# Performance work log

Measured on AMD Instinct MI355X. Metric: run time of the kernel, lower is better.

The kernel has to match this reference:

```python
import jax, jax.numpy as jnp
import numpy as np

DN = ('NCHW', 'OIHW', 'NCHW')
WINDOW_SIZES = (11, 25, 49)


def conv(x, w, b=None, pad=0, groups=1):
    y = jax.lax.conv_general_dilated(
        x, w, window_strides=(1, 1), padding=((pad, pad), (pad, pad)),
        dimension_numbers=DN, feature_group_count=groups)
    if b is not None:
        y = y + b[None, :, None, None]
    return y


def box_mean(f, wsize):
    # depthwise box-filter local mean with reflect padding (matches F.pad mode='reflect')
    C = f.shape[1]
    p = wsize // 2
    fp = jnp.pad(f, ((0, 0), (0, 0), (p, p), (p, p)), mode='reflect')
    k = jnp.ones((C, 1, wsize, wsize), f.dtype) / (wsize * wsize)
    return conv(fp, k, groups=C)


def std_map(features, wsize):
    # per-channel local std, channel-weighted sum, then **0.8
    C = features.shape[1]
    # C == 8 here, so weights are softmax(ones) == uniform (torch path for C != 4)
    cw = jax.nn.softmax(jnp.ones((C,), features.dtype))
    m = box_mean(features, wsize)
    m2 = box_mean(features ** 2, wsize)
    var = jnp.clip(m2 - m ** 2, 1e-6, None)
    res = jnp.sum(cw[None, :, None, None] * jnp.sqrt(var), axis=1, keepdims=True)
    return res ** 0.8  # [B,1,H,W]


def setup_inputs() -> dict:
    key = jax.random.key(0)
    ks = jax.random.split(key, 8)
    B, C, H, W = 8, 4, 512, 512
    x = jax.random.normal(ks[0], (B, C, H, W), dtype=jnp.float32)
    conv1_w = jax.random.normal(ks[1], (32, 4, 3, 3), dtype=jnp.float32) * 0.1
    conv1_b = jnp.zeros((32,), jnp.float32)
    conv2_w = jax.random.normal(ks[2], (16, 32, 3, 3), dtype=jnp.float32) * 0.05
    conv2_b = jnp.zeros((16,), jnp.float32)
    conv3_w = jax.random.normal(ks[3], (8, 16, 3, 3), dtype=jnp.float32) * 0.05
    conv3_b = jnp.zeros((8,), jnp.float32)
    # scale_fusion init: weight = 1/len(window_sizes), bias = 0
    fusion_w = jnp.full((1, len(WINDOW_SIZES), 1, 1), 1.0 / len(WINDOW_SIZES), jnp.float32)
    fusion_b = jnp.zeros((1,), jnp.float32)
    channel_weights = jnp.ones((4,), jnp.float32) / 4.0
    return dict(x=x, conv1_w=conv1_w, conv1_b=conv1_b, conv2_w=conv2_w,
                conv2_b=conv2_b, conv3_w=conv3_w, conv3_b=conv3_b,
                fusion_w=fusion_w, fusion_b=fusion_b,
                channel_weights=channel_weights)


def reference(x, conv1_w, conv1_b, conv2_w, conv2_b, conv3_w, conv3_b,
              fusion_w, fusion_b, channel_weights):
    lrelu = lambda v: jnp.where(v >= 0, v, 0.2 * v)
    # feature extractor: conv3x3 -> lrelu -> conv3x3 -> lrelu -> conv3x3
    f = lrelu(conv(x, conv1_w, conv1_b, pad=1))
    f = lrelu(conv(f, conv2_w, conv2_b, pad=1))
    f = conv(f, conv3_w, conv3_b, pad=1)  # [B,8,H,W]
    # multi-scale std maps
    maps = [std_map(f, w) for w in WINDOW_SIZES]
    multi = jnp.concatenate(maps, axis=1)  # [B,3,H,W]
    fused = jax.nn.relu(conv(multi, fusion_w, fusion_b, pad=0))  # [B,1,H,W]
    # adaptive thresholds (global quantiles over the whole fused std map)
    qs = jnp.quantile(fused.reshape(-1), jnp.array([0.25, 0.75], fused.dtype))
    q25, q75 = qs[0], qs[1]
    iqr = q75 - q25
    gstd = jnp.std(x, axis=(2, 3), keepdims=True, ddof=1)  # [B,4,1,1] (torch unbiased)
    lo = (q25 - 0.5 * iqr) * jnp.ones_like(gstd)
    hi = (q75 + 0.5 * iqr) * jnp.ones_like(gstd)
    gf = jnp.clip(gstd * 5.0, 0.5, 2.0)
    lo, hi = lo * gf, hi * gf
    cw = jax.nn.softmax(channel_weights)[None, :, None, None]
    cstd = jnp.std(x * cw, axis=(2, 3), keepdims=True, ddof=1)
    cf = jnp.clip(cstd * 2.0, 0.8, 1.2)
    lo, hi = lo * cf, hi * cf
    # mask generation: broadcast [B,1,H,W] vs [B,4,1,1] -> [B,4,H,W], then mean over C
    n = jnp.clip((fused - lo) / (hi - lo), 0.0, 1.0)
    mask = jax.nn.sigmoid(6.0 * n - 3.0)
    return jnp.mean(mask, axis=1, keepdims=True)  # [B,1,H,W]
```

## Files before the change

### kernel.cpp

```cpp
#include <hip/hip_runtime.h>
#include <cmath>

#define HH 512
#define WW 512
#define NB 8
#define CIN 4
#define C2 32
#define C3 16
#define CF 8
#define HW (HH*WW)
#define NPIX (NB*HW)
#define NBC 2

__device__ __forceinline__ float lrelu_f(float v){ return v < 0.f ? 0.2f*v : v; }
__device__ __forceinline__ int reflect_i(int i){ int r = i < 0 ? -i : i; return r >= HH ? 2*HH - 2 - r : r; }

template<int Ci, int Co, bool LRELU>
__global__ __launch_bounds__(256) void k_conv8(const float* __restrict__ in,
                                               const float* __restrict__ wgt,
                                               const float* __restrict__ bias,
                                               float* __restrict__ outp)
{
    constexpr int NG = Co/8;
    __shared__ float wl[Co*Ci*9];
    __shared__ float bl[Co];
    for (int i = threadIdx.x; i < Co*Ci*9; i += 256) wl[i] = wgt[i];
    if (threadIdx.x < Co) bl[threadIdx.x] = bias[threadIdx.x];
    __syncthreads();

    int bid   = blockIdx.x;
    int local = bid % (NG*128);
    int b     = bid / (NG*128);
    int cb    = local & 3;
    int rb    = (local >> 2) & 31;
    int cg    = local >> 7;
    int tid   = threadIdx.x;
    int col   = cb*128 + (tid & 31)*4;
    int row0  = rb*16  + (tid >> 5)*2;
    int co0   = cg*8;
    const float* inb = in + (size_t)b*Ci*HW;

    float acc[8][2][4];
    #pragma unroll
    for (int j=0;j<8;j++){
        float bv = bl[co0+j];
        #pragma unroll
        for (int r=0;r<2;r++)
            #pragma unroll
            for (int p=0;p<4;p++) acc[j][r][p] = bv;
    }

    #pragma unroll 2
    for (int ci=0; ci<Ci; ci++){
        float v[4][6];
        const float* inc = inb + (size_t)ci*HW;
        #pragma unroll
        for (int dy=0;dy<4;dy++){
            int hh = row0 + dy - 1;
            int hc = hh < 0 ? 0 : (hh > HH-1 ? HH-1 : hh);
            bool hok = (unsigned)hh < (unsigned)HH;
            #pragma unroll
            for (int dx=0;dx<6;dx++){
                int wx = col + dx - 1;
                int wc = wx < 0 ? 0 : (wx > WW-1 ? WW-1 : wx);
                float val = inc[hc*WW + wc];
                v[dy][dx] = (hok && (unsigned)wx < (unsigned)WW) ? val : 0.f;
            }
        }
        #pragma unroll
        for (int j=0;j<8;j++){
            const float* wr = &wl[((co0+j)*Ci + ci)*9];
            float wj[9];
            #pragma unroll
            for (int q=0;q<9;q++) wj[q] = wr[q];
            #pragma unroll
            for (int dy=0;dy<3;dy++){
                #pragma unroll
                for (int dx=0;dx<3;dx++){
                    float wv = wj[dy*3+dx];
                    #pragma unroll
                    for (int r=0;r<2;r++)
                        #pragma unroll
                        for (int p=0;p<4;p++)
                            acc[j][r][p] = fmaf(v[dy+r][dx+p], wv, acc[j][r][p]);
                }
            }
        }
    }

    float* ob = outp + (size_t)b*Co*HW;
    #pragma unroll
    for (int j=0;j<8;j++){
        #pragma unroll
        for (int r=0;r<2;r++){
            float4 o;
            o.x = LRELU ? lrelu_f(acc[j][r][0]) : acc[j][r][0];
            o.y = LRELU ? lrelu_f(acc[j][r][1]) : acc[j][r][1];
            o.z = LRELU ? lrelu_f(acc[j][r][2]) : acc[j][r][2];
            o.w = LRELU ? lrelu_f(acc[j][r][3]) : acc[j][r][3];
            *(float4*)(ob + (size_t)(co0+j)*HW + (size_t)(row0+r)*WW + col) = o;
        }
    }
}

template<int WS>
__global__ __launch_bounds__(256) void k_vbox(const float* __restrict__ f,
                                              float* __restrict__ vs,
                                              float* __restrict__ vq)
{
    constexpr int P = WS/2;
    constexpr int CH = 64;
    int bid   = blockIdx.x;
    int wb    = bid & 1;
    int hc    = (bid >> 1) & 7;
    int plane = bid >> 4;
    int w     = wb*256 + threadIdx.x;
    int h0    = hc*CH;
    const float* base = f  + (size_t)plane*HW + w;
    float*       os   = vs + (size_t)plane*HW + w;
    float*       oq   = vq + (size_t)plane*HW + w;

    float s = 0.f, q = 0.f;
    #pragma unroll
    for (int dy = -P; dy <= P; dy++){
        float v = base[(size_t)reflect_i(h0+dy)*WW];
        s += v; q = fmaf(v, v, q);
    }
    #pragma unroll 4
    for (int h = h0; h < h0+CH; h++){
        os[(size_t)h*WW] = s;
        oq[(size_t)h*WW] = q;
        float e = base[(size_t)reflect_i(h+1+P)*WW];
        float l = base[(size_t)reflect_i(h-P)*WW];
        s += e - l;
        q = fmaf(e, e, q);
        q = fmaf(-l, l, q);
    }
}

__device__ __forceinline__ int swz_i(int j){ return j + (j >> 4); }

template<int WS>
__global__ __launch_bounds__(256) void k_hbox(const float* __restrict__ vs,
                                              const float* __restrict__ vq,
                                              float* __restrict__ fused,
                                              const float* __restrict__ fwv, int sidx)
{
    constexpr int P   = WS/2;
    constexpr int L   = WW + 2*P;
    constexpr int SWL = L + (L >> 4) + 2;
    constexpr float inv = 1.f/((float)WS*(float)WS);
    __shared__ float sv[CF*SWL];
    __shared__ float sq[CF*SWL];

    int bid = blockIdx.x;
    int row = bid & (HH-1);
    int bb  = bid >> 9;
    const float* vsb = vs + ((size_t)bb*CF*HH + row)*WW;
    const float* vqb = vq + ((size_t)bb*CF*HH + row)*WW;

    for (int i = threadIdx.x; i < CF*L; i += 256){
        int c = i / L, j = i - c*L;
        int s = j - P; s = s < 0 ? -s : (s > WW-1 ? 2*WW-2 - s : s);
        sv[c*SWL + swz_i(j)] = vsb[(size_t)c*HW + s];
        sq[c*SWL + swz_i(j)] = vqb[(size_t)c*HW + s];
    }
    __syncthreads();

    int c = threadIdx.x >> 5;
    int g = threadIdx.x & 31;
    const float* pv = sv + c*SWL;
    const float* pq = sq + c*SWL;
    int bofs = 17*g;

    float S = 0.f, Q = 0.f;
    #pragma unroll
    for (int k = 0; k < WS; k++){
        S += pv[bofs + k + (k>>4)];
        Q += pq[bofs + k + (k>>4)];
    }
    float res[16];
    #pragma unroll
    for (int k = 0; k < 16; k++){
        float m  = S*inv;
        float m2 = Q*inv;
        float var = fmaxf(fmaf(-m, m, m2), 1e-6f);
        res[k] = sqrtf(var);
        if (k < 15){
            S += pv[bofs + (k+WS) + ((k+WS)>>4)] - pv[bofs + k + (k>>4)];
            Q += pq[bofs + (k+WS) + ((k+WS)>>4)] - pq[bofs + k + (k>>4)];
        }
    }
    __syncthreads();
    #pragma unroll
    for (int k = 0; k < 16; k++) sv[c*SWL + bofs + k + (k>>4)] = res[k];
    __syncthreads();

    float fwb = fwv[sidx];
    #pragma unroll
    for (int half = 0; half < 2; half++){
        int col = threadIdx.x + half*256;
        float a = 0.f;
        #pragma unroll
        for (int cc = 0; cc < CF; cc++) a += sv[cc*SWL + swz_i(col)];
        float val = powf(a*0.125f, 0.8f);
        fused[((size_t)bb*HH + row)*WW + col] += fwb*val;
    }
}

__global__ void k_h8(const float* __restrict__ fused, const float* __restrict__ fb,
                     unsigned* __restrict__ hist8)
{
    __shared__ unsigned lh[256];
    lh[threadIdx.x] = 0;
    __syncthreads();
    float fbv = fb[0];
    int i = blockIdx.x*256 + threadIdx.x;
    int stride = gridDim.x*256;
    for (; i < NPIX; i += stride){
        float v = fmaxf(fused[i] + fbv, 0.f);
        atomicAdd(&lh[__float_as_uint(v) >> 24], 1u);
    }
    __syncthreads();
    if (lh[threadIdx.x]) atomicAdd(&hist8[threadIdx.x], lh[threadIdx.x]);
}

__global__ void k_scan8(const unsigned* __restrict__ hist8,
                        int* __restrict__ cand8, int* __restrict__ rank8)
{
    if (threadIdx.x == 0){
        const unsigned RK[4] = {524287u, 524288u, 1572863u, 1572864u};
        unsigned cum = 0; int qi = 0;
        for (int b = 0; b < 256 && qi < 4; b++){
            unsigned cnt = hist8[b];
            while (qi < 4 && RK[qi] < cum + cnt){
                cand8[qi] = b; rank8[qi] = (int)(RK[qi] - cum); qi++;
            }
            cum += cnt;
        }
    }
}

__global__ void k_h8b(const float* __restrict__ fused, const float* __restrict__ fb,
                      const int* __restrict__ cand8, unsigned* __restrict__ hist8b)
{
    __shared__ unsigned lh[1024];
    for (int i = threadIdx.x; i < 1024; i += 256) lh[i] = 0;
    __syncthreads();
    float fbv = fb[0];
    int c0 = cand8[0], c1 = cand8[1], c2 = cand8[2], c3 = cand8[3];
    bool d1 = (c1 != c0);
    bool d2 = (c2 != c0) && (c2 != c1);
    bool d3 = (c3 != c0) && (c3 != c1) && (c3 != c2);
    int i = blockIdx.x*256 + threadIdx.x;
    int stride = gridDim.x*256;
    for (; i < NPIX; i += stride){
        unsigned u = __float_as_uint(fmaxf(fused[i] + fbv, 0.f));
        int hi = (int)(u >> 24);
        unsigned mid = (u >> 16) & 0xffu;
        if (hi == c0)       atomicAdd(&lh[mid],       1u);
        if (d1 && hi == c1) atomicAdd(&lh[256u+mid],  1u);
        if (d2 && hi == c2) atomicAdd(&lh[512u+mid],  1u);
        if (d3 && hi == c3) atomicAdd(&lh[768u+mid],  1u);
    }
    __syncthreads();
    for (int i = threadIdx.x; i < 1024; i += 256)
        if (lh[i]) atomicAdd(&hist8b[i], lh[i]);
}

__global__ void k_scan8b(const unsigned* __restrict__ hist8b,
                         const int* __restrict__ cand8, const int* __restrict__ rank8,
                         int* __restrict__ cand16, int* __restrict__ rank16)
{
    int qi = threadIdx.x;
    if (qi < 4){
        int slot = qi;
        for (int j = 0; j < qi; j++) if (cand8[j] == cand8[qi]){ slot = j; break; }
        const unsigned* h = hist8b + slot*256;
        unsigned k = (unsigned)rank8[qi], cum = 0;
        for (int b = 0; b < 256; b++){
            unsigned cnt = h[b];
            if (cnt && k >= cum && k < cum + cnt){
                cand16[qi] = (cand8[qi] << 8) | b;
                rank16[qi] = (int)(k - cum);
            }
            cum += cnt;
        }
    }
}

__global__ void k_h16(const float* __restrict__ fused, const float* __restrict__ fb,
                      const int* __restrict__ cand16, unsigned* __restrict__ histlo)
{
    float fbv = fb[0];
    int c0 = cand16[0], c1 = cand16[1], c2 = cand16[2], c3 = cand16[3];
    bool d1 = (c1 != c0);
    bool d2 = (c2 != c0) && (c2 != c1);
    bool d3 = (c3 != c0) && (c3 != c1) && (c3 != c2);
    int i = blockIdx.x*256 + threadIdx.x;
    int stride = gridDim.x*256;
    for (; i < NPIX; i += stride){
        unsigned u = __float_as_uint(fmaxf(fused[i] + fbv, 0.f));
        int hi = (int)(u >> 16);
        unsigned lo = u & 0xffffu;
        if (hi == c0)       atomicAdd(&histlo[lo],           1u);
        if (d1 && hi == c1) atomicAdd(&histlo[65536u + lo],  1u);
        if (d2 && hi == c2) atomicAdd(&histlo[131072u + lo], 1u);
        if (d3 && hi == c3) atomicAdd(&histlo[196608u + lo], 1u);
    }
}

__global__ void k_scan16(const unsigned* __restrict__ histlo,
                         const int* __restrict__ cand16, const int* __restrict__ rank16,
                         float* __restrict__ ostat)
{
    int qi = blockIdx.x;
    int slot = qi;
    for (int j = 0; j < qi; j++) if (cand16[j] == cand16[qi]){ slot = j; break; }
    const unsigned* hist = histlo + (size_t)slot*65536;
    __shared__ unsigned csum[256];
    __shared__ unsigned cbase[256];
    int t = threadIdx.x;
    unsigned s = 0;
    for (int i = 0; i < 256; i++) s += hist[t*256 + i];
    csum[t] = s;
    __syncthreads();
    if (t == 0){ unsigned run = 0; for (int i = 0; i < 256; i++){ cbase[i] = run; run += csum[i]; } }
    __syncthreads();
    unsigned k = (unsigned)rank16[qi];
    unsigned cum = cbase[t];
    for (int i = 0; i < 256; i++){
        unsigned cnt = hist[t*256 + i];
        if (cnt && k >= cum && k < cum + cnt)
            ostat[qi] = __uint_as_float(((unsigned)cand16[qi] << 16) | (unsigned)(t*256 + i));
        cum += cnt;
    }
}

__global__ void k_gstd_part(const float* __restrict__ x, double* __restrict__ part)
{
    int bid = blockIdx.x;
    int plane = bid >> 3, chunk = bid & 7;
    const float4* p4 = (const float4*)(x + (size_t)plane*HW + (size_t)chunk*32768);
    int t = threadIdx.x;
    double s=0.0, s2=0.0;
    for (int k=0;k<32;k++){
        float4 v = p4[k*256 + t];
        s  += (double)v.x + (double)v.y + (double)v.z + (double)v.w;
        s2 += (double)v.x*v.x + (double)v.y*v.y + (double)v.z*v.z + (double)v.w*v.w;
    }
    __shared__ double rs[256], rq[256];
    rs[t]=s; rq[t]=s2; __syncthreads();
    for (int off=128; off>0; off>>=1){
        if (t<off){ rs[t]+=rs[t+off]; rq[t]+=rq[t+off]; }
        __syncthreads();
    }
    if (t==0){ part[bid*2]=rs[0]; part[bid*2+1]=rq[0]; }
}

__global__ void k_gstd_final(const double* __restrict__ part, float* __restrict__ gstd)
{
    int t = threadIdx.x;
    if (t < 32){
        double s=0.0, s2=0.0;
        for (int j=0;j<8;j++){ s += part[(t*8+j)*2]; s2 += part[(t*8+j)*2+1]; }
        const double N = 262144.0;
        double var = (s2 - s*s/N) / (N - 1.0);
        gstd[t] = (float)sqrt(var < 0.0 ? 0.0 : var);
    }
}

__global__ void k_finalize(const float* __restrict__ ostat, const float* __restrict__ gstd,
                           const float* __restrict__ cwin, float* __restrict__ lov, float* __restrict__ hiv)
{
    int t = threadIdx.x;
    if (t < 32){
        float q25 = ostat[0] + 0.75f*(ostat[1]-ostat[0]);
        float q75 = ostat[2] + 0.25f*(ostat[3]-ostat[2]);
        float iqr = q75 - q25;
        float lo_b = q25 - 0.5f*iqr, hi_b = q75 + 0.5f*iqr;
        int c = t & 3;
        float m = fmaxf(fmaxf(cwin[0],cwin[1]), fmaxf(cwin[2],cwin[3]));
        float e0 = expf(cwin[0]-m), e1 = expf(cwin[1]-m), e2 = expf(cwin[2]-m), e3 = expf(cwin[3]-m);
        float smc = expf(cwin[c]-m) / (e0+e1+e2+e3);
        float g  = gstd[t];
        float gf = fminf(fmaxf(g*5.f, 0.5f), 2.f);
        float cf = fminf(fmaxf(smc*g*2.f, 0.8f), 1.2f);
        lov[t] = lo_b*gf*cf;
        hiv[t] = hi_b*gf*cf;
    }
}

__global__ void k_mask(const float* __restrict__ fused_in, const float* __restrict__ fb,
                       const float* __restrict__ lov, const float* __restrict__ hiv,
                       float* __restrict__ outp)
{
    int i = blockIdx.x*256 + threadIdx.x;
    float F = fmaxf(fused_in[i] + fb[0], 0.f);
    int b = i >> 18;
    float o = 0.f;
    #pragma unroll
    for (int c=0;c<4;c++){
        float lo = lov[b*4+c], hi = hiv[b*4+c];
        float n = (F - lo) / (hi - lo);
        n = fminf(fmaxf(n, 0.f), 1.f);
        o += 1.f/(1.f + expf(3.f - 6.f*n));
    }
    outp[i] = 0.25f * o;
}

extern "C" void kernel_launch(void* const* d_in, const int* in_sizes, int n_in,
                              void* d_out, int out_size, void* d_ws, size_t ws_size,
                              hipStream_t stream)
{
    const float* x  = (const float*)d_in[0];
    const float* w1 = (const float*)d_in[1];
    const float* b1 = (const float*)d_in[2];
    const float* w2 = (const float*)d_in[3];
    const float* b2 = (const float*)d_in[4];
    const float* w3 = (const float*)d_in[5];
    const float* b3 = (const float*)d_in[6];
    const float* fw = (const float*)d_in[7];
    const float* fb = (const float*)d_in[8];
    const float* cw = (const float*)d_in[9];
    float* out = (float*)d_out;
    char* ws = (char*)d_ws;

    size_t off = 0;
    auto take = [&](size_t bytes)->size_t{ size_t o = off; off += (bytes + 255) & ~(size_t)255; return o; };
    size_t o_h8     = take(256*4);
    size_t o_h8b    = take(1024*4);
    size_t o_histlo = take((size_t)4*65536*4);
    size_t o_c8     = take(4*4);
    size_t o_r8     = take(4*4);
    size_t o_c16    = take(4*4);
    size_t o_r16    = take(4*4);
    size_t o_os     = take(4*4);
    size_t o_part   = take(512*8);
    size_t o_gs     = take(32*4);
    size_t o_lo     = take(32*4);
    size_t o_hi     = take(32*4);
    size_t o_R1     = take((size_t)NB*C3*HW*4);
    size_t o_R2     = take((size_t)NBC*C2*HW*4);

    float*    f2buf  = (float*)(ws + o_R1);
    float*    vsb    = (float*)(ws + o_R1);
    float*    vqb    = vsb + (size_t)NB*CF*HW;
    float*    f1     = (float*)(ws + o_R2);
    float*    fbuf   = (float*)(ws + o_R2);
    unsigned* hist8  = (unsigned*)(ws + o_h8);
    unsigned* hist8b = (unsigned*)(ws + o_h8b);
    unsigned* histlo = (unsigned*)(ws + o_histlo);
    int*      c8     = (int*)(ws + o_c8);
    int*      r8     = (int*)(ws + o_r8);
    int*      c16    = (int*)(ws + o_c16);
    int*      r16    = (int*)(ws + o_r16);
    float*    osv    = (float*)(ws + o_os);
    double*   part   = (double*)(ws + o_part);
    float*    gs     = (float*)(ws + o_gs);
    float*    lov    = (float*)(ws + o_lo);
    float*    hiv    = (float*)(ws + o_hi);

    for (int ck = 0; ck < NB/NBC; ck++){
        const float* xb = x + (size_t)ck*NBC*CIN*HW;
        k_conv8<CIN,C2,true ><<<NBC*512,256,0,stream>>>(xb, w1, b1, f1);
        k_conv8<C2, C3,true ><<<NBC*256,256,0,stream>>>(f1, w2, b2,
                                                        f2buf + (size_t)ck*NBC*C3*HW);
    }
    k_conv8<C3, CF, false><<<NB*128,256,0,stream>>>(f2buf, w3, b3, fbuf);

    k_gstd_part<<<256,256,0,stream>>>(x, part);
    k_gstd_final<<<1,256,0,stream>>>(part, gs);

    hipMemsetAsync(out, 0, (size_t)NPIX*4, stream);
    const int vgrid = NB*CF*16, hgrid = NB*512;
    k_vbox<11><<<vgrid,256,0,stream>>>(fbuf, vsb, vqb);
    k_hbox<11><<<hgrid,256,0,stream>>>(vsb, vqb, out, fw, 0);
    k_vbox<25><<<vgrid,256,0,stream>>>(fbuf, vsb, vqb);
    k_hbox<25><<<hgrid,256,0,stream>>>(vsb, vqb, out, fw, 1);
    k_vbox<49><<<vgrid,256,0,stream>>>(fbuf, vsb, vqb);
    k_hbox<49><<<hgrid,256,0,stream>>>(vsb, vqb, out, fw, 2);

    hipMemsetAsync(hist8,  0, 256*4,  stream);
    hipMemsetAsync(hist8b, 0, 1024*4, stream);
    hipMemsetAsync(histlo, 0, (size_t)4*65536*4, stream);
    k_h8    <<<2048,256,0,stream>>>(out, fb, hist8);
    k_scan8 <<<1,64,0,stream>>>(hist8, c8, r8);
    k_h8b   <<<2048,256,0,stream>>>(out, fb, c8, hist8b);
    k_scan8b<<<1,64,0,stream>>>(hist8b, c8, r8, c16, r16);
    k_h16   <<<2048,256,0,stream>>>(out, fb, c16, histlo);
    k_scan16<<<4,256,0,stream>>>(histlo, c16, r16, osv);

    k_finalize<<<1,64,0,stream>>>(osv, gs, cw, lov, hiv);
    k_mask<<<NPIX/256,256,0,stream>>>(out, fb, lov, hiv, out);
}
```

Measured before the change: 916.7 us.

## Fuse vertical and horizontal box filters into one tiled kernel; shuffle conv halos

The separate vertical-sum and horizontal-sum kernels, which wrote intermediate vs/vq planes to global memory, are replaced by one kernel per window size. Each block owns a 16-row by 256-column band, keeps running vertical sums in registers and does the horizontal sliding sums from shared memory, so the large intermediate buffers and the output memset go away. The 3x3 conv input load now uses a float4 per row plus wave shuffles for the halo columns instead of six scalar loads. The trade-off is a small grid (512 blocks) with a __syncthreads-heavy per-row loop and uncoalesced reflected column gathers, which may reduce occupancy and parallelism.

```diff
diff --git a/kernel.cpp b/kernel.cpp
--- a/kernel.cpp
+++ b/kernel.cpp
@@ -35,7 +35,8 @@
     int rb    = (local >> 2) & 31;
     int cg    = local >> 7;
     int tid   = threadIdx.x;
-    int col   = cb*128 + (tid & 31)*4;
+    int lane  = tid & 31;
+    int col   = cb*128 + lane*4;
     int row0  = rb*16  + (tid >> 5)*2;
     int co0   = cg*8;
     const float* inb = in + (size_t)b*Ci*HW;
@@ -59,13 +60,18 @@
             int hh = row0 + dy - 1;
             int hc = hh < 0 ? 0 : (hh > HH-1 ? HH-1 : hh);
             bool hok = (unsigned)hh < (unsigned)HH;
-            #pragma unroll
-            for (int dx=0;dx<6;dx++){
-                int wx = col + dx - 1;
-                int wc = wx < 0 ? 0 : (wx > WW-1 ? WW-1 : wx);
-                float val = inc[hc*WW + wc];
-                v[dy][dx] = (hok && (unsigned)wx < (unsigned)WW) ? val : 0.f;
-            }
+            const float* rowp = inc + hc*WW;
+            float4 m = *(const float4*)(rowp + col);
+            float lft = 0.f, rgt = 0.f;
+            if (lane == 0  && col > 0)      lft = rowp[col-1];
+            if (lane == 31 && col+4 < WW)   rgt = rowp[col+4];
+            float v0 = __shfl_up(m.w, 1, 32);
+            float v5 = __shfl_down(m.x, 1, 32);
+            if (lane == 0)  v0 = lft;
+            if (lane == 31) v5 = rgt;
+            if (!hok){ m.x=0.f; m.y=0.f; m.z=0.f; m.w=0.f; v0=0.f; v5=0.f; }
+            v[dy][0]=v0; v[dy][1]=m.x; v[dy][2]=m.y;
+            v[dy][3]=m.z; v[dy][4]=m.w; v[dy][5]=v5;
         }
         #pragma unroll
         for (int j=0;j<8;j++){
@@ -103,108 +109,113 @@
     }
 }
 
-template<int WS>
-__global__ __launch_bounds__(256) void k_vbox(const float* __restrict__ f,
-                                              float* __restrict__ vs,
-                                              float* __restrict__ vq)
-{
-    constexpr int P = WS/2;
-    constexpr int CH = 64;
-    int bid   = blockIdx.x;
-    int wb    = bid & 1;
-    int hc    = (bid >> 1) & 7;
-    int plane = bid >> 4;
-    int w     = wb*256 + threadIdx.x;
-    int h0    = hc*CH;
-    const float* base = f  + (size_t)plane*HW + w;
-    float*       os   = vs + (size_t)plane*HW + w;
-    float*       oq   = vq + (size_t)plane*HW + w;
-
-    float s = 0.f, q = 0.f;
+template<int WS, bool FIRST>
+__global__ __launch_bounds__(256) void k_vhbox(const float* __restrict__ f,
+                                               float* __restrict__ fused,
+                                               const float* __restrict__ fwv, int sidx)
+{
+    constexpr int P    = WS/2;
+    constexpr int SW   = ((256 + 2*P + 31)/32)*32;
+    constexpr int SEGC = SW/32;
+    constexpr int SVW  = (SW + (SW>>4) + 3) | 1;
+    constexpr int RSW  = 256 + 16 + 2;
+    constexpr float inv = 1.f/((float)WS*(float)WS);
+
+    __shared__ float sv[CF*SVW];
+    __shared__ float sq[CF*SVW];
+    __shared__ float resv[CF*RSW];
+
+    int bid  = blockIdx.x;
+    int band = bid & 31;
+    int half = (bid >> 5) & 1;
+    int b    = bid >> 6;
+    int r0   = band*16;
+    int c0   = half*256;
+    int tid  = threadIdx.x;
+    int ch   = tid >> 5;
+    int seg  = tid & 31;
+
+    const float* fp = f + (size_t)(b*CF + ch)*HW;
+
+    int rc[SEGC];
     #pragma unroll
+    for (int k = 0; k < SEGC; k++){
+        int gc = c0 - P + k*32 + seg;
+        gc = gc < 0 ? -gc : (gc > WW-1 ? 2*WW-2 - gc : gc);
+        rc[k] = gc;
+    }
+
+    float vsr[SEGC], vqr[SEGC];
+    #pragma unroll
+    for (int k = 0; k < SEGC; k++){ vsr[k]=0.f; vqr[k]=0.f; }
     for (int dy = -P; dy <= P; dy++){
-        float v = base[(size_t)reflect_i(h0+dy)*WW];
-        s += v; q = fmaf(v, v, q);
-    }
-    #pragma unroll 4
-    for (int h = h0; h < h0+CH; h++){
-        os[(size_t)h*WW] = s;
-        oq[(size_t)h*WW] = q;
-        float e = base[(size_t)reflect_i(h+1+P)*WW];
-        float l = base[(size_t)reflect_i(h-P)*WW];
-        s += e - l;
-        q = fmaf(e, e, q);
-        q = fmaf(-l, l, q);
-    }
-}
-
-__device__ __forceinline__ int swz_i(int j){ return j + (j >> 4); }
-
-template<int WS>
-__global__ __launch_bounds__(256) void k_hbox(const float* __restrict__ vs,
-                                              const float* __restrict__ vq,
-                                              float* __restrict__ fused,
-                                              const float* __restrict__ fwv, int sidx)
-{
-    constexpr int P   = WS/2;
-    constexpr int L   = WW + 2*P;
-    constexpr int SWL = L + (L >> 4) + 2;
-    constexpr float inv = 1.f/((float)WS*(float)WS);
-    __shared__ float sv[CF*SWL];
-    __shared__ float sq[CF*SWL];
-
-    int bid = blockIdx.x;
-    int row = bid & (HH-1);
-    int bb  = bid >> 9;
-    const float* vsb = vs + ((size_t)bb*CF*HH + row)*WW;
-    const float* vqb = vq + ((size_t)bb*CF*HH + row)*WW;
-
-    for (int i = threadIdx.x; i < CF*L; i += 256){
-        int c = i / L, j = i - c*L;
-        int s = j - P; s = s < 0 ? -s : (s > WW-1 ? 2*WW-2 - s : s);
-        sv[c*SWL + swz_i(j)] = vsb[(size_t)c*HW + s];
-        sq[c*SWL + swz_i(j)] = vqb[(size_t)c*HW + s];
-    }
-    __syncthreads();
-
-    int c = threadIdx.x >> 5;
-    int g = threadIdx.x & 31;
-    const float* pv = sv + c*SWL;
-    const float* pq = sq + c*SWL;
-    int bofs = 17*g;
-
-    float S = 0.f, Q = 0.f;
-    #pragma unroll
-    for (int k = 0; k < WS; k++){
-        S += pv[bofs + k + (k>>4)];
-        Q += pq[bofs + k + (k>>4)];
-    }
-    float res[16];
-    #pragma unroll
-    for (int k = 0; k < 16; k++){
-        float m  = S*inv;
-        float m2 = Q*inv;
-        float var = fmaxf(fmaf(-m, m, m2), 1e-6f);
-        res[k] = sqrtf(var);
-        if (k < 15){
-            S += pv[bofs + (k+WS) + ((k+WS)>>4)] - pv[bofs + k + (k>>4)];
-            Q += pq[bofs + (k+WS) + ((k+WS)>>4)] - pq[bofs + k + (k>>4)];
-        }
-    }
-    __syncthreads();
-    #pragma unroll
-    for (int k = 0; k < 16; k++) sv[c*SWL + bofs + k + (k>>4)] = res[k];
-    __syncthreads();
+        const float* rp = fp + (size_t)reflect_i(r0+dy)*WW;
+        #pragma unroll
+        for (int k = 0; k < SEGC; k++){
+            float v = rp[rc[k]];
+            vsr[k] += v; vqr[k] = fmaf(v, v, vqr[k]);
+        }
+    }
 
     float fwb = fwv[sidx];
-    #pragma unroll
-    for (int half = 0; half < 2; half++){
-        int col = threadIdx.x + half*256;
+
+    for (int rr = 0; rr < 16; rr++){
+        __syncthreads();
+        #pragma unroll
+        for (int k = 0; k < SEGC; k++){
+            int j = k*32 + seg; int sj = j + (j>>4);
+            sv[ch*SVW + sj] = vsr[k];
+            sq[ch*SVW + sj] = vqr[k];
+        }
+        float ev[SEGC], lv[SEGC];
+        if (rr < 15){
+            const float* ep = fp + (size_t)reflect_i(r0+rr+1+P)*WW;
+            const float* lp = fp + (size_t)reflect_i(r0+rr-P)*WW;
+            #pragma unroll
+            for (int k = 0; k < SEGC; k++){ ev[k]=ep[rc[k]]; lv[k]=lp[rc[k]]; }
+        }
+        __syncthreads();
+        int oc0 = seg*8;
+        float S = 0.f, Q = 0.f;
+        #pragma unroll
+        for (int k = 0; k < WS; k++){
+            int j = oc0 + k; int sj = j + (j>>4);
+            S += sv[ch*SVW + sj];
+            Q += sq[ch*SVW + sj];
+        }
+        float res[8];
+        #pragma unroll
+        for (int t = 0; t < 8; t++){
+            float m  = S*inv, m2 = Q*inv;
+            float var = fmaxf(fmaf(-m, m, m2), 1e-6f);
+            res[t] = sqrtf(var);
+            if (t < 7){
+                int ja = oc0 + t + WS, jb = oc0 + t;
+                S += sv[ch*SVW + ja + (ja>>4)] - sv[ch*SVW + jb + (jb>>4)];
+                Q += sq[ch*SVW + ja + (ja>>4)] - sq[ch*SVW + jb + (jb>>4)];
+            }
+        }
+        #pragma unroll
+        for (int t = 0; t < 8; t++){
+            int j = oc0 + t;
+            resv[ch*RSW + j + (j>>4)] = res[t];
+        }
+        if (rr < 15){
+            #pragma unroll
+            for (int k = 0; k < SEGC; k++){
+                vsr[k] += ev[k] - lv[k];
+                vqr[k] = fmaf(ev[k], ev[k], vqr[k]);
+                vqr[k] = fmaf(-lv[k], lv[k], vqr[k]);
+            }
+        }
+        __syncthreads();
+        int colI = tid;
         float a = 0.f;
         #pragma unroll
-        for (int cc = 0; cc < CF; cc++) a += sv[cc*SWL + swz_i(col)];
-        float val = powf(a*0.125f, 0.8f);
-        fused[((size_t)bb*HH + row)*WW + col] += fwb*val;
+        for (int cc = 0; cc < CF; cc++) a += resv[cc*RSW + colI + (colI>>4)];
+        float val = fwb * powf(a*0.125f, 0.8f);
+        size_t oi = ((size_t)b*HH + r0 + rr)*WW + c0 + colI;
+        if (FIRST) fused[oi] = val; else fused[oi] += val;
     }
 }
 
@@ -444,8 +455,6 @@
     size_t o_R2     = take((size_t)NBC*C2*HW*4);
 
     float*    f2buf  = (float*)(ws + o_R1);
-    float*    vsb    = (float*)(ws + o_R1);
-    float*    vqb    = vsb + (size_t)NB*CF*HW;
     float*    f1     = (float*)(ws + o_R2);
     float*    fbuf   = (float*)(ws + o_R2);
     unsigned* hist8  = (unsigned*)(ws + o_h8);
@@ -472,14 +481,10 @@
     k_gstd_part<<<256,256,0,stream>>>(x, part);
     k_gstd_final<<<1,256,0,stream>>>(part, gs);
 
-    hipMemsetAsync(out, 0, (size_t)NPIX*4, stream);
-    const int vgrid = NB*CF*16, hgrid = NB*512;
-    k_vbox<11><<<vgrid,256,0,stream>>>(fbuf, vsb, vqb);
-    k_hbox<11><<<hgrid,256,0,stream>>>(vsb, vqb, out, fw, 0);
-    k_vbox<25><<<vgrid,256,0,stream>>>(fbuf, vsb, vqb);
-    k_hbox<25><<<hgrid,256,0,stream>>>(vsb, vqb, out, fw, 1);
-    k_vbox<49><<<vgrid,256,0,stream>>>(fbuf, vsb, vqb);
-    k_hbox<49><<<hgrid,256,0,stream>>>(vsb, vqb, out, fw, 2);
+    const int bgrid = NB*2*32;
+    k_vhbox<11,true ><<<bgrid,256,0,stream>>>(fbuf, out, fw, 0);
+    k_vhbox<25,false><<<bgrid,256,0,stream>>>(fbuf, out, fw, 1);
+    k_vhbox<49,false><<<bgrid,256,0,stream>>>(fbuf, out, fw, 2);
 
     hipMemsetAsync(hist8,  0, 256*4,  stream);
     hipMemsetAsync(hist8b, 0, 1024*4, stream);
```

Result: no change. 905.9 us (-1.2%).
